# Kernel tuning notes

Hardware: AMD Instinct MI355X
Metric: run time of the kernel (lower is better)

The kernel has to match this reference:

```python
import jax, jax.numpy as jnp
import numpy as np

B, GL, GF, N = 4, 4, 128, 1024
CS, CN, NA = 32, 16, 16
S, HS = 512, 512


def squash(s, axis):
    # mag_sq/(1+mag_sq) * s/mag == s * mag/(1+mag_sq)
    mag_sq = jnp.sum(s * s, axis=axis, keepdims=True)
    return s * (jnp.sqrt(mag_sq) / (1.0 + mag_sq))


def routing(u_hat, n_iter=3):
    # u_hat: [M, I, J, U]; dynamic routing, softmax over J, squash over J (as in source)
    M, I, J, U = u_hat.shape
    b = jnp.zeros((I, J), dtype=u_hat.dtype)
    v = None
    for _ in range(n_iter):
        c = jax.nn.softmax(b, axis=1)                       # [I, J]
        s = jnp.einsum('ij,miju->mju', c, u_hat)            # [M, J, U]
        v = squash(s, axis=1)                               # squash over J (torch dim=2)
        b = b + jnp.einsum('miju,mju->mij', u_hat, v).mean(axis=0)
    return v


def setup_inputs():
    key = jax.random.key(0)
    ks = jax.random.split(key, 7)
    sc = 0.1
    return {
        'graph_embed': jax.random.normal(ks[0], (B, GL, GF, N), jnp.float32),
        'hidden': jax.random.normal(ks[1], (B, S, HS), jnp.float32),
        'Wp': jax.random.normal(ks[2], (GL, CS, GL, GF), jnp.float32) * sc,  # per-unit conv kernels
        'bp': jax.random.normal(ks[3], (GL, CS), jnp.float32) * sc,
        'Wg': jax.random.normal(ks[4], (CS, CN, CS, GL), jnp.float32) * sc,  # graph caps [I,J,U,K]
        'Wa': jax.random.normal(ks[5], (CS + HS,), jnp.float32) * sc,        # attention_1 weight
        'Ws': jax.random.normal(ks[6], (CN, NA, CS, CS), jnp.float32) * sc,  # aspect caps [I,J,U,K]
    }


def _per_example(x, h, Wp, bp, Wg, Wa, Ws):
    # x: [GL, GF, N], h: [S, HS]
    gl, gf, n = x.shape
    # primary capsules: each unit's conv kernel covers all (GL,GF) -> full contraction
    u = jnp.einsum('uclf,lfn->ucn', Wp, x) + bp[:, :, None]   # [GL, CS, N]
    u = squash(u.reshape(gl, -1), axis=1)                     # squash over CS*N (torch dim=2)
    p = u.reshape(n, gl, CS)                                  # torch .view(-1, GL, CS)
    # graph capsule routing
    u_hat_g = jnp.einsum('ijuk,mik->miju', Wg, p.transpose(0, 2, 1))  # [N, CS, CN, CS]
    v_g = routing(u_hat_g)                                    # [N, CN, CS]
    g = v_g.reshape(n, CS, CN).mean(axis=0).reshape(CN, CS)   # torch .view semantics
    # adaptive attention: Linear([g;h]) with no bias, softmax over capsules
    score = jax.nn.softmax((g @ Wa[:CS])[None, :] + (h @ Wa[CS:])[:, None], axis=1)  # [S, CN]
    condensed = g[None, :, :] * score[:, :, None]             # [S, CN, CS]
    # aspect capsule routing (transpose(1,2) then layer-internal transpose cancel out)
    u_hat_a = jnp.einsum('ijuk,mik->miju', Ws, condensed)     # [S, CN, NA, CS]
    return routing(u_hat_a)                                   # [S, NA, CS]


def reference(graph_embed, hidden, Wp, bp, Wg, Wa, Ws):
    f = jax.vmap(_per_example, in_axes=(0, 0, None, None, None, None, None))
    return f(graph_embed, hidden, Wp, bp, Wg, Wa, Ws)   # [B, S, NA, CS]
```

## Files before the change

kernel.cpp:

```cpp
#include <hip/hip_runtime.h>
#include <math.h>


static constexpr int OFF_U   = 0;
static constexpr int OFF_S   = 524288;
static constexpr int OFF_SSP = 2621440;
static constexpr int OFF_BGP = 2621696;
static constexpr int OFF_GP  = 2654464;
static constexpr int OFF_VA  = 2687232;
static constexpr int OFF_MS  = 2689280;
static constexpr int OFF_UH  = 2820352;
static constexpr int OFF_WGR = 2853120;

__global__ void k_primary_part(const float* __restrict__ X, const float* __restrict__ Wp,
                               float* __restrict__ Upart,
                               const float* __restrict__ Wg, float* __restrict__ Wgr)
{
    __shared__ float Wt[128 * 68];
    const int t = threadIdx.x;
    if (blockIdx.z == 16) {
        const int blk = blockIdx.x * 16 + blockIdx.y;
#pragma unroll
        for (int r = 0; r < 8; ++r) {
            const int e = blk * 2048 + r * 256 + t;
            const int q = e >> 9, rem = e & 511;
            const int u = rem >> 4, j = rem & 15;
            const int i = q & 31, kk = q >> 5;
            Wgr[e] = Wg[((i * 16 + j) * 32 + u) * 4 + kk];
        }
        return;
    }
    const int ct = blockIdx.x, nt = blockIdx.y;
    const int b = blockIdx.z >> 2, ks = blockIdx.z & 3;
    const int tn = t & 15, tc = t >> 4;
    const int c0 = ct * 64, n0 = nt * 64;
#pragma unroll
    for (int i = 0; i < 8; ++i) {
        const int idx = t + i * 256;
        const int c = idx >> 5, k4 = idx & 31;
        const float4 wv = *(const float4*)&Wp[(size_t)(c0 + c) * 512 + ks * 128 + k4 * 4];
        Wt[(k4 * 4 + 0) * 68 + c] = wv.x;
        Wt[(k4 * 4 + 1) * 68 + c] = wv.y;
        Wt[(k4 * 4 + 2) * 68 + c] = wv.z;
        Wt[(k4 * 4 + 3) * 68 + c] = wv.w;
    }
    __syncthreads();
    float acc[4][4] = {};
    const float* Xp = X + (size_t)b * 524288 + (size_t)(ks * 128) * 1024 + n0 + tn * 4;
#pragma unroll 4
    for (int k = 0; k < 128; ++k) {
        const float4 xv = *(const float4*)(Xp + (size_t)k * 1024);
        const float4 wv = *(const float4*)&Wt[k * 68 + tc * 4];
        const float w[4] = {wv.x, wv.y, wv.z, wv.w};
        const float x[4] = {xv.x, xv.y, xv.z, xv.w};
#pragma unroll
        for (int ci = 0; ci < 4; ++ci)
#pragma unroll
            for (int ni = 0; ni < 4; ++ni)
                acc[ci][ni] = fmaf(w[ci], x[ni], acc[ci][ni]);
    }
    float* up = Upart + (size_t)ks * 524288 + (size_t)b * 131072;
#pragma unroll
    for (int ci = 0; ci < 4; ++ci)
        *(float4*)&up[(size_t)(c0 + tc * 4 + ci) * 1024 + n0 + tn * 4] =
            make_float4(acc[ci][0], acc[ci][1], acc[ci][2], acc[ci][3]);
}

__global__ void k_reduceU(const float* __restrict__ Upart, const float* __restrict__ bp,
                          float* __restrict__ U, float* __restrict__ SSp)
{
    __shared__ float red[256];
    const int blk = blockIdx.x, t = threadIdx.x;
    const int b = blk >> 5, cg = blk & 31;
    float ssq = 0.f;
#pragma unroll
    for (int i = 0; i < 4; ++i) {
        const int c = cg * 4 + i;
        const int f4 = b * 32768 + c * 256 + t;
        float4 s = ((const float4*)Upart)[f4];
#pragma unroll
        for (int ks = 1; ks < 4; ++ks) {
            const float4 p = ((const float4*)Upart)[ks * 131072 + f4];
            s.x += p.x; s.y += p.y; s.z += p.z; s.w += p.w;
        }
        const float bv = bp[c];
        s.x += bv; s.y += bv; s.z += bv; s.w += bv;
        ssq = fmaf(s.x, s.x, ssq); ssq = fmaf(s.y, s.y, ssq);
        ssq = fmaf(s.z, s.z, ssq); ssq = fmaf(s.w, s.w, ssq);
        ((float4*)U)[f4] = s;
    }
    red[t] = ssq;
    __syncthreads();
    for (int s = 128; s > 0; s >>= 1) {
        if (t < s) red[t] += red[t + s];
        __syncthreads();
    }
    if (t == 0) SSp[(b * 4 + (cg >> 3)) * 8 + (cg & 7)] = red[0];
}

__global__ __launch_bounds__(256) void k_smatmulM2(
    const float* __restrict__ U, const float* __restrict__ SSp,
    const float* __restrict__ Bgp, const float* __restrict__ Wgr,
    float* __restrict__ S, float* __restrict__ MS, float* __restrict__ Gp,
    const int bg0)
{
    __shared__ __align__(16) float Pt[64 * 68];
    __shared__ __align__(16) float Ct[64 * 160];
    __shared__ float cls[512];
    __shared__ float bgs[512];
    __shared__ float gacc[128];
    const int mt = blockIdx.x, us = blockIdx.y, b = blockIdx.z;
    const int t = threadIdx.x;
    const int tm = t >> 4;
    const int uu = t & 7, jh = (t >> 3) & 1;
    const int m0 = mt * 64;

    if (bg0) {
        cls[t] = 0.0625f;
        cls[t + 256] = 0.0625f;
    } else {
#pragma unroll
        for (int h = 0; h < 2; ++h) {
            const int p = t + h * 256;
            const int i = p >> 4, j = p & 15;
            float s = 0.f;
#pragma unroll 4
            for (int mc = 0; mc < 16; ++mc)
                s += Bgp[((b * 16 + mc) * 8 + (j >> 1)) * 64 + i * 2 + (j & 1)];
            bgs[p] = s * (1.f / 1024.f);
        }
        __syncthreads();
        if (t < 32) {
            float vals[16];
            float mx = -1e30f;
            for (int j = 0; j < 16; ++j) { vals[j] = bgs[t * 16 + j]; mx = fmaxf(mx, vals[j]); }
            float sum = 0.f;
            for (int j = 0; j < 16; ++j) { vals[j] = expf(vals[j] - mx); sum += vals[j]; }
            const float inv = 1.f / sum;
            for (int j = 0; j < 16; ++j) cls[t * 16 + j] = vals[j] * inv;
        }
    }
    if (Gp != nullptr && t < 128) gacc[t] = 0.f;
    float ssum = 0.f;
#pragma unroll
    for (int i = 0; i < 8; ++i) ssum += SSp[(b * 4 + (mt >> 2)) * 8 + i];
    const float sc = sqrtf(ssum) / (1.f + ssum);
    float acc[4][8] = {};
    const float* Ub = U + (size_t)b * 131072 + (size_t)m0 * 128;
    __syncthreads();

    for (int kc = 0; kc < 2; ++kc) {
#pragma unroll
        for (int it = 0; it < 4; ++it) {
            const int x = t + it * 256;
            const int m = x & 63, q4 = x >> 6;
            const float4 v = *(const float4*)&Ub[(size_t)m * 128 + kc * 64 + q4 * 4];
            Pt[(q4 * 4 + 0) * 68 + m] = v.x * sc;
            Pt[(q4 * 4 + 1) * 68 + m] = v.y * sc;
            Pt[(q4 * 4 + 2) * 68 + m] = v.z * sc;
            Pt[(q4 * 4 + 3) * 68 + m] = v.w * sc;
        }
#pragma unroll
        for (int it = 0; it < 8; ++it) {
            const int x = t + it * 256;
            const int c4 = (x & 31) * 4, qL = x >> 5;
            const int q = kc * 64 + qL;
            const int i = q & 31;
            const int j0 = c4 & 15;
            const float4 w = *(const float4*)&Wgr[(size_t)q * 512 + us * 128 + c4];
            const int cp = qL * 160 + c4 + ((c4 >> 4) << 2);
            Ct[cp + 0] = cls[i * 16 + j0 + 0] * w.x;
            Ct[cp + 1] = cls[i * 16 + j0 + 1] * w.y;
            Ct[cp + 2] = cls[i * 16 + j0 + 2] * w.z;
            Ct[cp + 3] = cls[i * 16 + j0 + 3] * w.w;
        }
        __syncthreads();
        const int cbase = uu * 20 + jh * 8;
#pragma unroll 4
        for (int qL = 0; qL < 64; ++qL) {
            const float4 p4 = *(const float4*)&Pt[qL * 68 + tm * 4];
            const float4 ca = *(const float4*)&Ct[qL * 160 + cbase];
            const float4 cb = *(const float4*)&Ct[qL * 160 + cbase + 4];
            const float pm[4] = {p4.x, p4.y, p4.z, p4.w};
            const float cj[8] = {ca.x, ca.y, ca.z, ca.w, cb.x, cb.y, cb.z, cb.w};
#pragma unroll
            for (int mm = 0; mm < 4; ++mm)
#pragma unroll
                for (int jj = 0; jj < 8; ++jj)
                    acc[mm][jj] = fmaf(pm[mm], cj[jj], acc[mm][jj]);
        }
        __syncthreads();
    }

#pragma unroll
    for (int mm = 0; mm < 4; ++mm) {
        float* Sp = S + (size_t)b * 524288 + (size_t)(m0 + tm * 4 + mm) * 512 + us * 8 + uu;
#pragma unroll
        for (int jj = 0; jj < 8; ++jj)
            Sp[(jh * 8 + jj) * 32] = acc[mm][jj];
    }

    if (Gp == nullptr) {
#pragma unroll
        for (int mm = 0; mm < 4; ++mm) {
            float msq = 0.f;
#pragma unroll
            for (int jj = 0; jj < 8; ++jj) msq = fmaf(acc[mm][jj], acc[mm][jj], msq);
            msq += __shfl_xor(msq, 8);
            if (jh == 0)
                MS[b * 32768 + (m0 + tm * 4 + mm) * 32 + us * 8 + uu] =
                    sqrtf(msq) / (1.f + msq);
        }
    } else {
        float part[8];
#pragma unroll
        for (int jj = 0; jj < 8; ++jj) part[jj] = 0.f;
#pragma unroll
        for (int mm = 0; mm < 4; ++mm) {
            float msq = 0.f;
#pragma unroll
            for (int jj = 0; jj < 8; ++jj) msq = fmaf(acc[mm][jj], acc[mm][jj], msq);
            msq += __shfl_xor(msq, 8);
            const float msc = sqrtf(msq) / (1.f + msq);
#pragma unroll
            for (int jj = 0; jj < 8; ++jj) part[jj] = fmaf(acc[mm][jj], msc, part[jj]);
        }
#pragma unroll
        for (int jj = 0; jj < 8; ++jj)
            atomicAdd(&gacc[(jh * 8 + jj) * 8 + uu], part[jj]);
        __syncthreads();
        if (t < 128) {
            const int j = t >> 3, u2 = t & 7;
            Gp[(size_t)(b * 16 + mt) * 512 + j * 32 + us * 8 + u2] =
                gacc[t] * (1.f / 1024.f);
        }
    }
}

__global__ void k_tbu2(const float* __restrict__ U, const float* __restrict__ SSp,
                       const float* __restrict__ S, const float* __restrict__ MS,
                       const float* __restrict__ Wg, float* __restrict__ Bgp,
                       const int first)
{
    __shared__ float Ps[64 * 132];
    __shared__ float Vs[64 * 68];
    __shared__ float bup[64];
    const int jt = blockIdx.x, mc = blockIdx.y, b = blockIdx.z;
    const int t = threadIdx.x;
    const int tq = t & 31, tjv = t >> 5;
    const int m0 = mc * 64;
    if (t < 64) bup[t] = 0.f;
    float ssum = 0.f;
#pragma unroll
    for (int i = 0; i < 8; ++i) ssum += SSp[(b * 4 + (mc >> 2)) * 8 + i];
    const float sc = sqrtf(ssum) / (1.f + ssum);
#pragma unroll
    for (int i = 0; i < 8; ++i) {
        const int f4 = t + i * 256;
        const int r = f4 >> 5, q4 = f4 & 31;
        float4 v = *(const float4*)&U[(size_t)b * 131072 + (size_t)(m0 + r) * 128 + q4 * 4];
        v.x *= sc; v.y *= sc; v.z *= sc; v.w *= sc;
        *(float4*)&Ps[r * 132 + q4 * 4] = v;
    }
#pragma unroll
    for (int i = 0; i < 4; ++i) {
        const int f4 = t + i * 256;
        const int r = f4 >> 4, c4 = f4 & 15;
        const int m = m0 + r;
        float4 v = *(const float4*)&S[(size_t)b * 524288 + (size_t)m * 512 + jt * 64 + c4 * 4];
        const int ub = (c4 * 4) & 31;
        const float* msp = MS + b * 32768 + m * 32;
        v.x *= msp[ub + 0]; v.y *= msp[ub + 1]; v.z *= msp[ub + 2]; v.w *= msp[ub + 3];
        *(float4*)&Vs[r * 68 + c4 * 4] = v;
    }
    __syncthreads();
    float acc[4][8] = {};
#pragma unroll 2
    for (int m = 0; m < 64; ++m) {
        const float4 p4 = *(const float4*)&Ps[m * 132 + tq * 4];
        const float4 va = *(const float4*)&Vs[m * 68 + tjv * 8];
        const float4 vb = *(const float4*)&Vs[m * 68 + tjv * 8 + 4];
        const float pv[4] = {p4.x, p4.y, p4.z, p4.w};
        const float vv[8] = {va.x, va.y, va.z, va.w, vb.x, vb.y, vb.z, vb.w};
#pragma unroll
        for (int qi = 0; qi < 4; ++qi)
#pragma unroll
            for (int ji = 0; ji < 8; ++ji)
                acc[qi][ji] = fmaf(pv[qi], vv[ji], acc[qi][ji]);
    }
    const int k = tq >> 3;
    const int j_loc = tjv >> 2;
    const int j = jt * 2 + j_loc;
    const int u0 = (tjv & 3) * 8;
#pragma unroll
    for (int qi = 0; qi < 4; ++qi) {
        const int i = (tq & 7) * 4 + qi;
        const float* wp = Wg + ((i * 16 + j) * 32) * 4 + k;
        float s = 0.f;
#pragma unroll
        for (int ji = 0; ji < 8; ++ji)
            s = fmaf(wp[(u0 + ji) * 4], acc[qi][ji], s);
        s += __shfl_xor(s, 8);
        s += __shfl_xor(s, 16);
        s += __shfl_xor(s, 32);
        if ((t & 56) == 0) atomicAdd(&bup[i * 2 + j_loc], s);
    }
    __syncthreads();
    if (t < 64) {
        float* slot = &Bgp[((b * 16 + mc) * 8 + jt) * 64 + t];
        if (first) *slot = bup[t];
        else       *slot += bup[t];
    }
}

__global__ void k_uhat2(const float* __restrict__ Gp, const float* __restrict__ Wa,
                        const float* __restrict__ Ws, float* __restrict__ UH)
{
    const int b = blockIdx.y;
    const int t = threadIdx.x;
    __shared__ float g[512], cond[512], score[16], red[16];
    float g0 = 0.f, g1 = 0.f;
#pragma unroll 4
    for (int mt = 0; mt < 16; ++mt) {
        const float* gp = Gp + (size_t)(b * 16 + mt) * 512;
        g0 += gp[t];
        g1 += gp[t + 256];
    }
    g[t] = g0;
    g[t + 256] = g1;
    __syncthreads();
    if (t < 16) {
        float s = 0.f;
        for (int u = 0; u < 32; ++u) s = fmaf(g[t * 32 + u], Wa[u], s);
        red[t] = s;
    }
    __syncthreads();
    if (t == 0) {
        float mx = -1e30f;
        for (int j = 0; j < 16; ++j) mx = fmaxf(mx, red[j]);
        float sum = 0.f;
        for (int j = 0; j < 16; ++j) { score[j] = expf(red[j] - mx); sum += score[j]; }
        const float inv = 1.f / sum;
        for (int j = 0; j < 16; ++j) score[j] *= inv;
    }
    __syncthreads();
    cond[t] = g[t] * score[t >> 5];
    cond[t + 256] = g[t + 256] * score[(t + 256) >> 5];
    __syncthreads();
    const int e0 = blockIdx.x * 1024 + t * 4;
    const int i = e0 >> 9;
    const float* cp = cond + i * 32;
    const float* wp = Ws + (size_t)e0 * 32;
    float res[4];
#pragma unroll
    for (int jj = 0; jj < 4; ++jj) {
        float s = 0.f;
#pragma unroll
        for (int k8 = 0; k8 < 8; ++k8) {
            const float4 w = *(const float4*)(wp + jj * 32 + k8 * 4);
            s = fmaf(w.x, cp[k8 * 4 + 0], s);
            s = fmaf(w.y, cp[k8 * 4 + 1], s);
            s = fmaf(w.z, cp[k8 * 4 + 2], s);
            s = fmaf(w.w, cp[k8 * 4 + 3], s);
        }
        res[jj] = s;
    }
    ((float4*)UH)[(b * 8192 + e0) >> 2] = make_float4(res[0], res[1], res[2], res[3]);
}

__global__ void k_route(const float* __restrict__ UH, float* __restrict__ VA)
{
    const int b = blockIdx.x;
    const int t = threadIdx.x;
    __shared__ float uh[8192], ba[256], cc[256], sbuf[512], msc[32];
#pragma unroll
    for (int i = 0; i < 8; ++i)
        ((float4*)uh)[i * 256 + t] = ((const float4*)UH)[b * 2048 + i * 256 + t];
    ba[t] = 0.f;
    __syncthreads();
    for (int it = 0; it < 3; ++it) {
        if (t < 16) {
            float mx = -1e30f;
            for (int j = 0; j < 16; ++j) mx = fmaxf(mx, ba[t * 16 + j]);
            float sum = 0.f;
            for (int j = 0; j < 16; ++j) { cc[t * 16 + j] = expf(ba[t * 16 + j] - mx); sum += cc[t * 16 + j]; }
            const float inv = 1.f / sum;
            for (int j = 0; j < 16; ++j) cc[t * 16 + j] *= inv;
        }
        __syncthreads();
        for (int h = 0; h < 2; ++h) {
            const int e = h * 256 + t;
            const int j = e >> 5;
            float s = 0.f;
            for (int i = 0; i < 16; ++i) s = fmaf(cc[i * 16 + j], uh[i * 512 + e], s);
            sbuf[e] = s;
        }
        __syncthreads();
        if (t < 32) {
            float mg = 0.f;
            for (int j = 0; j < 16; ++j) { const float x = sbuf[j * 32 + t]; mg = fmaf(x, x, mg); }
            msc[t] = sqrtf(mg) / (1.f + mg);
        }
        __syncthreads();
        for (int h = 0; h < 2; ++h) {
            const int e = h * 256 + t;
            sbuf[e] *= msc[e & 31];
        }
        __syncthreads();
        if (it < 2) {
            const int i = t >> 4, j = t & 15;
            float s = 0.f;
            for (int u = 0; u < 32; ++u) s = fmaf(uh[i * 512 + j * 32 + u], sbuf[j * 32 + u], s);
            ba[t] += s;
            __syncthreads();
        }
    }
    VA[b * 512 + t] = sbuf[t];
    VA[b * 512 + 256 + t] = sbuf[256 + t];
}

__global__ void k_out(const float* __restrict__ VA, float* __restrict__ out)
{
    const int idx = blockIdx.x * 256 + threadIdx.x;
    const int b = idx >> 16;
    const int jv4 = idx & 127;
    ((float4*)out)[idx] = ((const float4*)VA)[b * 128 + jv4];
}

extern "C" void kernel_launch(void* const* d_in, const int* in_sizes, int n_in,
                              void* d_out, int out_size, void* d_ws, size_t ws_size,
                              hipStream_t stream)
{
    const float* X   = (const float*)d_in[0];
    const float* Wp  = (const float*)d_in[2];
    const float* bp  = (const float*)d_in[3];
    const float* Wg  = (const float*)d_in[4];
    const float* Wa  = (const float*)d_in[5];
    const float* Wsp = (const float*)d_in[6];
    float* out = (float*)d_out;
    float* ws = (float*)d_ws;

    float* U   = ws + OFF_U;
    float* S   = ws + OFF_S;
    float* SSp = ws + OFF_SSP;
    float* Bgp = ws + OFF_BGP;
    float* Gp  = ws + OFF_GP;
    float* VA  = ws + OFF_VA;
    float* MS  = ws + OFF_MS;
    float* UH  = ws + OFF_UH;
    float* Wgr = ws + OFF_WGR;


    k_primary_part<<<dim3(2, 16, 17), 256, 0, stream>>>(X, Wp, S, Wg, Wgr);
    k_reduceU<<<128, 256, 0, stream>>>(S, bp, U, SSp);

    k_smatmulM2<<<dim3(16, 4, 4), 256, 0, stream>>>(U, SSp, Bgp, Wgr, S, MS, nullptr, 1);
    k_tbu2<<<dim3(8, 16, 4), 256, 0, stream>>>(U, SSp, S, MS, Wg, Bgp, 1);
    k_smatmulM2<<<dim3(16, 4, 4), 256, 0, stream>>>(U, SSp, Bgp, Wgr, S, MS, nullptr, 0);
    k_tbu2<<<dim3(8, 16, 4), 256, 0, stream>>>(U, SSp, S, MS, Wg, Bgp, 0);
    k_smatmulM2<<<dim3(16, 4, 4), 256, 0, stream>>>(U, SSp, Bgp, Wgr, S, nullptr, Gp, 0);

    k_uhat2<<<dim3(8, 4), 256, 0, stream>>>(Gp, Wa, Wsp, UH);
    k_route<<<4, 256, 0, stream>>>(UH, VA);
    k_out<<<1024, 256, 0, stream>>>(VA, out);
}
```

Measured before the change: 196.3 us.

## Fuse routing agreement update into s-matmul kernel, eliminating S and MS round-trips

Merges the separate agreement-update kernel into the s-computation kernel. The squashed v tile now stays in shared memory and is contracted with the re-staged primary capsules and Wgr inside the same block. Per-block partial b updates go to a new Bgp2 buffer that the next iteration sums over 64 partials. This removes writing and re-reading the large S and MS intermediates and two launches per routing pass. In exchange each block does extra work, uses more registers for the 4x16 accumulator, and reads more partials at the start of each iteration.

Measured after the change: 195.9 us. No clear change (-0.2%).

```diff
diff --git a/kernel.cpp b/kernel.cpp
--- a/kernel.cpp
+++ b/kernel.cpp
@@ -2,15 +2,14 @@
 #include <math.h>
 
 
-static constexpr int OFF_U   = 0;
-static constexpr int OFF_S   = 524288;
-static constexpr int OFF_SSP = 2621440;
-static constexpr int OFF_BGP = 2621696;
-static constexpr int OFF_GP  = 2654464;
-static constexpr int OFF_VA  = 2687232;
-static constexpr int OFF_MS  = 2689280;
-static constexpr int OFF_UH  = 2820352;
-static constexpr int OFF_WGR = 2853120;
+static constexpr int OFF_U    = 0;
+static constexpr int OFF_UPART= 524288;
+static constexpr int OFF_SSP  = 2621440;
+static constexpr int OFF_BGP2 = 2621696;
+static constexpr int OFF_GP   = 2752768;
+static constexpr int OFF_VA   = 2785536;
+static constexpr int OFF_UH   = 2787584;
+static constexpr int OFF_WGR  = 2820352;
 
 __global__ void k_primary_part(const float* __restrict__ X, const float* __restrict__ Wp,
                                float* __restrict__ Upart,
@@ -98,16 +97,16 @@
     if (t == 0) SSp[(b * 4 + (cg >> 3)) * 8 + (cg & 7)] = red[0];
 }
 
-__global__ __launch_bounds__(256) void k_smatmulM2(
+__global__ __launch_bounds__(256) void k_iter(
     const float* __restrict__ U, const float* __restrict__ SSp,
-    const float* __restrict__ Bgp, const float* __restrict__ Wgr,
-    float* __restrict__ S, float* __restrict__ MS, float* __restrict__ Gp,
-    const int bg0)
+    float* __restrict__ Bgp2, const float* __restrict__ Wgr,
+    float* __restrict__ Gp, const int first, const int last)
 {
     __shared__ __align__(16) float Pt[64 * 68];
-    __shared__ __align__(16) float Ct[64 * 160];
+    __shared__ __align__(16) float CtVs[64 * 160];
     __shared__ float cls[512];
     __shared__ float bgs[512];
+    __shared__ float bup[512];
     __shared__ float gacc[128];
     const int mt = blockIdx.x, us = blockIdx.y, b = blockIdx.z;
     const int t = threadIdx.x;
@@ -115,18 +114,17 @@
     const int uu = t & 7, jh = (t >> 3) & 1;
     const int m0 = mt * 64;
 
-    if (bg0) {
+    if (first) {
         cls[t] = 0.0625f;
         cls[t + 256] = 0.0625f;
     } else {
 #pragma unroll
         for (int h = 0; h < 2; ++h) {
             const int p = t + h * 256;
-            const int i = p >> 4, j = p & 15;
+            const float* bp2 = Bgp2 + (size_t)b * 32768 + p;
             float s = 0.f;
-#pragma unroll 4
-            for (int mc = 0; mc < 16; ++mc)
-                s += Bgp[((b * 16 + mc) * 8 + (j >> 1)) * 64 + i * 2 + (j & 1)];
+#pragma unroll 8
+            for (int g = 0; g < 64; ++g) s += bp2[g * 512];
             bgs[p] = s * (1.f / 1024.f);
         }
         __syncthreads();
@@ -140,7 +138,7 @@
             for (int j = 0; j < 16; ++j) cls[t * 16 + j] = vals[j] * inv;
         }
     }
-    if (Gp != nullptr && t < 128) gacc[t] = 0.f;
+    if (last && t < 128) gacc[t] = 0.f;
     float ssum = 0.f;
 #pragma unroll
     for (int i = 0; i < 8; ++i) ssum += SSp[(b * 4 + (mt >> 2)) * 8 + i];
@@ -169,18 +167,18 @@
             const int j0 = c4 & 15;
             const float4 w = *(const float4*)&Wgr[(size_t)q * 512 + us * 128 + c4];
             const int cp = qL * 160 + c4 + ((c4 >> 4) << 2);
-            Ct[cp + 0] = cls[i * 16 + j0 + 0] * w.x;
-            Ct[cp + 1] = cls[i * 16 + j0 + 1] * w.y;
-            Ct[cp + 2] = cls[i * 16 + j0 + 2] * w.z;
-            Ct[cp + 3] = cls[i * 16 + j0 + 3] * w.w;
+            CtVs[cp + 0] = cls[i * 16 + j0 + 0] * w.x;
+            CtVs[cp + 1] = cls[i * 16 + j0 + 1] * w.y;
+            CtVs[cp + 2] = cls[i * 16 + j0 + 2] * w.z;
+            CtVs[cp + 3] = cls[i * 16 + j0 + 3] * w.w;
         }
         __syncthreads();
         const int cbase = uu * 20 + jh * 8;
 #pragma unroll 4
         for (int qL = 0; qL < 64; ++qL) {
             const float4 p4 = *(const float4*)&Pt[qL * 68 + tm * 4];
-            const float4 ca = *(const float4*)&Ct[qL * 160 + cbase];
-            const float4 cb = *(const float4*)&Ct[qL * 160 + cbase + 4];
+            const float4 ca = *(const float4*)&CtVs[qL * 160 + cbase];
+            const float4 cb = *(const float4*)&CtVs[qL * 160 + cbase + 4];
             const float pm[4] = {p4.x, p4.y, p4.z, p4.w};
             const float cj[8] = {ca.x, ca.y, ca.z, ca.w, cb.x, cb.y, cb.z, cb.w};
 #pragma unroll
@@ -192,39 +190,24 @@
         __syncthreads();
     }
 
+    float msc[4];
 #pragma unroll
     for (int mm = 0; mm < 4; ++mm) {
-        float* Sp = S + (size_t)b * 524288 + (size_t)(m0 + tm * 4 + mm) * 512 + us * 8 + uu;
-#pragma unroll
-        for (int jj = 0; jj < 8; ++jj)
-            Sp[(jh * 8 + jj) * 32] = acc[mm][jj];
-    }
-
-    if (Gp == nullptr) {
-#pragma unroll
-        for (int mm = 0; mm < 4; ++mm) {
-            float msq = 0.f;
-#pragma unroll
-            for (int jj = 0; jj < 8; ++jj) msq = fmaf(acc[mm][jj], acc[mm][jj], msq);
-            msq += __shfl_xor(msq, 8);
-            if (jh == 0)
-                MS[b * 32768 + (m0 + tm * 4 + mm) * 32 + us * 8 + uu] =
-                    sqrtf(msq) / (1.f + msq);
-        }
-    } else {
+        float msq = 0.f;
+#pragma unroll
+        for (int jj = 0; jj < 8; ++jj) msq = fmaf(acc[mm][jj], acc[mm][jj], msq);
+        msq += __shfl_xor(msq, 8);
+        msc[mm] = sqrtf(msq) / (1.f + msq);
+    }
+
+    if (last) {
         float part[8];
 #pragma unroll
         for (int jj = 0; jj < 8; ++jj) part[jj] = 0.f;
 #pragma unroll
-        for (int mm = 0; mm < 4; ++mm) {
-            float msq = 0.f;
-#pragma unroll
-            for (int jj = 0; jj < 8; ++jj) msq = fmaf(acc[mm][jj], acc[mm][jj], msq);
-            msq += __shfl_xor(msq, 8);
-            const float msc = sqrtf(msq) / (1.f + msq);
-#pragma unroll
-            for (int jj = 0; jj < 8; ++jj) part[jj] = fmaf(acc[mm][jj], msc, part[jj]);
-        }
+        for (int mm = 0; mm < 4; ++mm)
+#pragma unroll
+            for (int jj = 0; jj < 8; ++jj) part[jj] = fmaf(acc[mm][jj], msc[mm], part[jj]);
 #pragma unroll
         for (int jj = 0; jj < 8; ++jj)
             atomicAdd(&gacc[(jh * 8 + jj) * 8 + uu], part[jj]);
@@ -234,82 +217,70 @@
             Gp[(size_t)(b * 16 + mt) * 512 + j * 32 + us * 8 + u2] =
                 gacc[t] * (1.f / 1024.f);
         }
-    }
-}
-
-__global__ void k_tbu2(const float* __restrict__ U, const float* __restrict__ SSp,
-                       const float* __restrict__ S, const float* __restrict__ MS,
-                       const float* __restrict__ Wg, float* __restrict__ Bgp,
-                       const int first)
-{
-    __shared__ float Ps[64 * 132];
-    __shared__ float Vs[64 * 68];
-    __shared__ float bup[64];
-    const int jt = blockIdx.x, mc = blockIdx.y, b = blockIdx.z;
-    const int t = threadIdx.x;
+        return;
+    }
+
+    float* Vs = CtVs;
+#pragma unroll
+    for (int mm = 0; mm < 4; ++mm)
+#pragma unroll
+        for (int jj = 0; jj < 8; ++jj)
+            Vs[(tm * 4 + mm) * 132 + jh * 64 + jj * 8 + uu] = acc[mm][jj] * msc[mm];
+
     const int tq = t & 31, tjv = t >> 5;
-    const int m0 = mc * 64;
-    if (t < 64) bup[t] = 0.f;
-    float ssum = 0.f;
-#pragma unroll
-    for (int i = 0; i < 8; ++i) ssum += SSp[(b * 4 + (mc >> 2)) * 8 + i];
-    const float sc = sqrtf(ssum) / (1.f + ssum);
-#pragma unroll
-    for (int i = 0; i < 8; ++i) {
-        const int f4 = t + i * 256;
-        const int r = f4 >> 5, q4 = f4 & 31;
-        float4 v = *(const float4*)&U[(size_t)b * 131072 + (size_t)(m0 + r) * 128 + q4 * 4];
-        v.x *= sc; v.y *= sc; v.z *= sc; v.w *= sc;
-        *(float4*)&Ps[r * 132 + q4 * 4] = v;
-    }
-#pragma unroll
-    for (int i = 0; i < 4; ++i) {
-        const int f4 = t + i * 256;
-        const int r = f4 >> 4, c4 = f4 & 15;
-        const int m = m0 + r;
-        float4 v = *(const float4*)&S[(size_t)b * 524288 + (size_t)m * 512 + jt * 64 + c4 * 4];
-        const int ub = (c4 * 4) & 31;
-        const float* msp = MS + b * 32768 + m * 32;
-        v.x *= msp[ub + 0]; v.y *= msp[ub + 1]; v.z *= msp[ub + 2]; v.w *= msp[ub + 3];
-        *(float4*)&Vs[r * 68 + c4 * 4] = v;
-    }
-    __syncthreads();
-    float acc[4][8] = {};
+    float acc2[4][16] = {};
+    for (int kc = 0; kc < 2; ++kc) {
+        __syncthreads();
+#pragma unroll
+        for (int it = 0; it < 4; ++it) {
+            const int x = t + it * 256;
+            const int m = x & 63, q4 = x >> 6;
+            const float4 v = *(const float4*)&Ub[(size_t)m * 128 + kc * 64 + q4 * 4];
+            Pt[(q4 * 4 + 0) * 68 + m] = v.x * sc;
+            Pt[(q4 * 4 + 1) * 68 + m] = v.y * sc;
+            Pt[(q4 * 4 + 2) * 68 + m] = v.z * sc;
+            Pt[(q4 * 4 + 3) * 68 + m] = v.w * sc;
+        }
+        __syncthreads();
 #pragma unroll 2
-    for (int m = 0; m < 64; ++m) {
-        const float4 p4 = *(const float4*)&Ps[m * 132 + tq * 4];
-        const float4 va = *(const float4*)&Vs[m * 68 + tjv * 8];
-        const float4 vb = *(const float4*)&Vs[m * 68 + tjv * 8 + 4];
-        const float pv[4] = {p4.x, p4.y, p4.z, p4.w};
-        const float vv[8] = {va.x, va.y, va.z, va.w, vb.x, vb.y, vb.z, vb.w};
-#pragma unroll
-        for (int qi = 0; qi < 4; ++qi)
-#pragma unroll
-            for (int ji = 0; ji < 8; ++ji)
-                acc[qi][ji] = fmaf(pv[qi], vv[ji], acc[qi][ji]);
-    }
-    const int k = tq >> 3;
-    const int j_loc = tjv >> 2;
-    const int j = jt * 2 + j_loc;
-    const int u0 = (tjv & 3) * 8;
-#pragma unroll
-    for (int qi = 0; qi < 4; ++qi) {
-        const int i = (tq & 7) * 4 + qi;
-        const float* wp = Wg + ((i * 16 + j) * 32) * 4 + k;
+        for (int m = 0; m < 64; ++m) {
+            const float p0 = Pt[tq * 68 + m];
+            const float p1 = Pt[(tq + 32) * 68 + m];
+            const float4 v0 = *(const float4*)&Vs[m * 132 + tjv * 16];
+            const float4 v1 = *(const float4*)&Vs[m * 132 + tjv * 16 + 4];
+            const float4 v2 = *(const float4*)&Vs[m * 132 + tjv * 16 + 8];
+            const float4 v3 = *(const float4*)&Vs[m * 132 + tjv * 16 + 12];
+            const float vv[16] = {v0.x, v0.y, v0.z, v0.w, v1.x, v1.y, v1.z, v1.w,
+                                  v2.x, v2.y, v2.z, v2.w, v3.x, v3.y, v3.z, v3.w};
+#pragma unroll
+            for (int ji = 0; ji < 16; ++ji) {
+                acc2[2 * kc + 0][ji] = fmaf(p0, vv[ji], acc2[2 * kc + 0][ji]);
+                acc2[2 * kc + 1][ji] = fmaf(p1, vv[ji], acc2[2 * kc + 1][ji]);
+            }
+        }
+    }
+#pragma unroll
+    for (int jl = 0; jl < 2; ++jl) {
+        const int j = tjv * 2 + jl;
         float s = 0.f;
 #pragma unroll
-        for (int ji = 0; ji < 8; ++ji)
-            s = fmaf(wp[(u0 + ji) * 4], acc[qi][ji], s);
-        s += __shfl_xor(s, 8);
-        s += __shfl_xor(s, 16);
-        s += __shfl_xor(s, 32);
-        if ((t & 56) == 0) atomicAdd(&bup[i * 2 + j_loc], s);
-    }
-    __syncthreads();
-    if (t < 64) {
-        float* slot = &Bgp[((b * 16 + mc) * 8 + jt) * 64 + t];
-        if (first) *slot = bup[t];
-        else       *slot += bup[t];
+        for (int k = 0; k < 4; ++k) {
+            const float* wr = Wgr + (size_t)(k * 32 + tq) * 512 + us * 128 + j;
+#pragma unroll
+            for (int ue = 0; ue < 8; ++ue)
+                s = fmaf(wr[ue * 16], acc2[k][jl * 8 + ue], s);
+        }
+        bup[tq * 16 + j] = s;
+    }
+    __syncthreads();
+    {
+        float* base = Bgp2 + (size_t)b * 32768 + (size_t)(mt * 4 + us) * 512;
+#pragma unroll
+        for (int h = 0; h < 2; ++h) {
+            const int p = t + h * 256;
+            if (first) base[p] = bup[p];
+            else       base[p] += bup[p];
+        }
     }
 }
 
@@ -440,25 +411,21 @@
     float* out = (float*)d_out;
     float* ws = (float*)d_ws;
 
-    float* U   = ws + OFF_U;
-    float* S   = ws + OFF_S;
-    float* SSp = ws + OFF_SSP;
-    float* Bgp = ws + OFF_BGP;
-    float* Gp  = ws + OFF_GP;
-    float* VA  = ws + OFF_VA;
-    float* MS  = ws + OFF_MS;
-    float* UH  = ws + OFF_UH;
-    float* Wgr = ws + OFF_WGR;
-
-
-    k_primary_part<<<dim3(2, 16, 17), 256, 0, stream>>>(X, Wp, S, Wg, Wgr);
-    k_reduceU<<<128, 256, 0, stream>>>(S, bp, U, SSp);
-
-    k_smatmulM2<<<dim3(16, 4, 4), 256, 0, stream>>>(U, SSp, Bgp, Wgr, S, MS, nullptr, 1);
-    k_tbu2<<<dim3(8, 16, 4), 256, 0, stream>>>(U, SSp, S, MS, Wg, Bgp, 1);
-    k_smatmulM2<<<dim3(16, 4, 4), 256, 0, stream>>>(U, SSp, Bgp, Wgr, S, MS, nullptr, 0);
-    k_tbu2<<<dim3(8, 16, 4), 256, 0, stream>>>(U, SSp, S, MS, Wg, Bgp, 0);
-    k_smatmulM2<<<dim3(16, 4, 4), 256, 0, stream>>>(U, SSp, Bgp, Wgr, S, nullptr, Gp, 0);
+    float* U    = ws + OFF_U;
+    float* Up   = ws + OFF_UPART;
+    float* SSp  = ws + OFF_SSP;
+    float* Bgp2 = ws + OFF_BGP2;
+    float* Gp   = ws + OFF_GP;
+    float* VA   = ws + OFF_VA;
+    float* UH   = ws + OFF_UH;
+    float* Wgr  = ws + OFF_WGR;
+
+    k_primary_part<<<dim3(2, 16, 17), 256, 0, stream>>>(X, Wp, Up, Wg, Wgr);
+    k_reduceU<<<128, 256, 0, stream>>>(Up, bp, U, SSp);
+
+    k_iter<<<dim3(16, 4, 4), 256, 0, stream>>>(U, SSp, Bgp2, Wgr, nullptr, 1, 0);
+    k_iter<<<dim3(16, 4, 4), 256, 0, stream>>>(U, SSp, Bgp2, Wgr, nullptr, 0, 0);
+    k_iter<<<dim3(16, 4, 4), 256, 0, stream>>>(U, SSp, Bgp2, Wgr, Gp, 0, 1);
 
     k_uhat2<<<dim3(8, 4), 256, 0, stream>>>(Gp, Wa, Wsp, UH);
     k_route<<<4, 256, 0, stream>>>(UH, VA);
```
